# Optimization experiments

Measured on AMD Instinct MI355X. Metric: run time of the kernel, lower is better.

Reference implementation:

```python
import jax, jax.numpy as jnp
import numpy as np

B_, T_, IDIM, D, H, FF, L, MAXLEN = 8, 512, 1799, 256, 4, 2048, 16, 1000
DK = D // H


def _ln(x, g, b, eps=1e-12):
    m = jnp.mean(x, axis=-1, keepdims=True)
    v = jnp.mean((x - m) ** 2, axis=-1, keepdims=True)
    return (x - m) * jax.lax.rsqrt(v + eps) * g + b


def setup_inputs() -> dict:
    key = jax.random.key(0)
    ks = jax.random.split(key, 16)
    s = 0.02
    n = lambda k, shape: jax.random.normal(k, shape, jnp.float32) * s
    return {
        'xs': jax.random.normal(ks[0], (B_, T_, IDIM), jnp.float32),
        'masks': jnp.ones((B_, 1, T_), jnp.int32),
        'emb_w': n(ks[1], (D, IDIM)), 'emb_b': jnp.zeros((D,), jnp.float32),
        'emb_g': jnp.ones((D,), jnp.float32), 'emb_beta': jnp.zeros((D,), jnp.float32),
        'pe_k': n(ks[2], (2 * MAXLEN, DK)),
        'Wq': n(ks[3], (L, D, D)), 'bq': jnp.zeros((L, D), jnp.float32),
        'Wk': n(ks[4], (L, D, D)), 'bk': jnp.zeros((L, D), jnp.float32),
        'Wv': n(ks[5], (L, D, D)), 'bv': jnp.zeros((L, D), jnp.float32),
        'Wo': n(ks[6], (L, D, D)), 'bo': jnp.zeros((L, D), jnp.float32),
        'ln1_g': jnp.ones((L, D), jnp.float32), 'ln1_b': jnp.zeros((L, D), jnp.float32),
        'ln2_g': jnp.ones((L, D), jnp.float32), 'ln2_b': jnp.zeros((L, D), jnp.float32),
        'lnk_g': jnp.ones((L, DK), jnp.float32), 'lnk_b': jnp.zeros((L, DK), jnp.float32),
        'W1': n(ks[7], (L, FF, D)), 'b1': jnp.zeros((L, FF), jnp.float32),
        'W2': n(ks[8], (L, D, FF)), 'b2': jnp.zeros((L, D), jnp.float32),
        'after_g': jnp.ones((D,), jnp.float32), 'after_b': jnp.zeros((D,), jnp.float32),
    }


def reference(xs, masks, emb_w, emb_b, emb_g, emb_beta, pe_k, Wq, bq, Wk, bk, Wv, bv, Wo, bo,
              ln1_g, ln1_b, ln2_g, ln2_b, lnk_g, lnk_b, W1, b1, W2, b2, after_g, after_b):
    # embed: Linear -> LayerNorm -> (Dropout=id) -> ReLU
    x = jax.nn.relu(_ln(xs @ emb_w.T + emb_b, emb_g, emb_beta))  # [B,T,D]
    # relative position table gather: pos_k [T,T,DK]
    pos = jnp.arange(T_)
    rel = jnp.clip(pos[:, None] - pos[None, :], -MAXLEN, MAXLEN - 1) + MAXLEN
    pos_k = pe_k[rel]
    neg = (masks == 0)[:, None, :, :]  # [B,1,1,T]
    minval = jnp.finfo(x.dtype).min
    scale = 1.0 / np.sqrt(DK).astype(np.float32)

    def block(x, p):
        y = _ln(x, p['ln1_g'], p['ln1_b'])
        pk = _ln(pos_k, p['lnk_g'], p['lnk_b'])  # norm_k applied per layer
        proj = lambda W, b: (y @ W.T + b).reshape(B_, T_, H, DK).transpose(0, 2, 1, 3)
        q = proj(p['Wq'], p['bq'])  # [B,H,T,DK]
        k = proj(p['Wk'], p['bk'])
        v = proj(p['Wv'], p['bv'])
        A = jnp.einsum('bhtd,bhsd->bhts', q, k)
        Bt = jnp.einsum('bhtd,tsd->bhts', q, pk)  # rel-pos bias term
        scores = jnp.where(neg, minval, (A + Bt) * scale)
        attn = jnp.where(neg, 0.0, jax.nn.softmax(scores, axis=-1))
        o = jnp.einsum('bhts,bhsd->bhtd', attn, v)
        o = o.transpose(0, 2, 1, 3).reshape(B_, T_, D)
        x = x + o @ p['Wo'].T + p['bo']
        y2 = _ln(x, p['ln2_g'], p['ln2_b'])
        ff = jax.nn.relu(y2 @ p['W1'].T + p['b1']) @ p['W2'].T + p['b2']
        return x + ff, None

    params = {'Wq': Wq, 'bq': bq, 'Wk': Wk, 'bk': bk, 'Wv': Wv, 'bv': bv, 'Wo': Wo, 'bo': bo,
              'ln1_g': ln1_g, 'ln1_b': ln1_b, 'ln2_g': ln2_g, 'ln2_b': ln2_b,
              'lnk_g': lnk_g, 'lnk_b': lnk_b, 'W1': W1, 'b1': b1, 'W2': W2, 'b2': b2}
    x, _ = jax.lax.scan(block, x, params)
    return _ln(x, after_g, after_b)
```

## Files before the change

### kernel.cpp

```cpp
#include <hip/hip_runtime.h>
#include <cstdint>


typedef __bf16 bf16_t;
typedef bf16_t bf16x4 __attribute__((ext_vector_type(4)));
typedef bf16_t bf16x8 __attribute__((ext_vector_type(8)));
typedef float  f32x4  __attribute__((ext_vector_type(4)));

#define B_    8
#define T_    512
#define IDIM  1799
#define KPAD  1856
#define D_    256
#define H_    4
#define DK    64
#define FF_   2048
#define L_    16
#define NROW  4096
#define PKROWS 2000
#define NBH   32
#define NSA   4

__device__ __forceinline__ f32x4 mfma16(bf16x8 a, bf16x8 b, f32x4 c) {
  return __builtin_amdgcn_mfma_f32_16x16x32_bf16(a, b, c, 0, 0, 0);
}

__device__ __forceinline__ void async_cp16(const void* g, void* l) {
  __builtin_amdgcn_global_load_lds(
      (__attribute__((address_space(1))) void*)(g),
      (__attribute__((address_space(3))) void*)(l), 16, 0, 0);
}

#define WCAT_N (L_ * 768 * 256)
#define WOB_N  (L_ * 256 * 256)
#define W1B_N  (L_ * 2048 * 256)
#define W2B_N  (L_ * 256 * 2048)
#define BCAT_N (L_ * 768)
#define PREP_TOT (WCAT_N + WOB_N + W1B_N + W2B_N + BCAT_N)

__global__ __launch_bounds__(256) void prep_all(
    const float* __restrict__ wq, const float* __restrict__ wk,
    const float* __restrict__ wv, const float* __restrict__ wo,
    const float* __restrict__ w1, const float* __restrict__ w2,
    const float* __restrict__ bq, const float* __restrict__ bk,
    const float* __restrict__ bv, bf16_t* __restrict__ wcat,
    bf16_t* __restrict__ wob, bf16_t* __restrict__ w1b,
    bf16_t* __restrict__ w2b, float* __restrict__ bcat) {
  const int stride = gridDim.x * 256;
  for (int i = blockIdx.x * 256 + threadIdx.x; i < PREP_TOT; i += stride) {
    int j = i;
    if (j < WCAT_N) {
      const int per_l = 768 * 256;
      int l = j / per_l, r = j - l * per_l;
      int n = r >> 8, c = r & 255;
      int sel = n >> 8, nn = n & 255;
      const float* wsrc = (sel == 0) ? wq : (sel == 1) ? wk : wv;
      wcat[j] = (bf16_t)wsrc[((size_t)l * 256 + nn) * 256 + c];
      continue;
    }
    j -= WCAT_N;
    if (j < WOB_N) { wob[j] = (bf16_t)wo[j]; continue; }
    j -= WOB_N;
    if (j < W1B_N) { w1b[j] = (bf16_t)w1[j]; continue; }
    j -= W1B_N;
    if (j < W2B_N) { w2b[j] = (bf16_t)w2[j]; continue; }
    j -= W2B_N;
    {
      int l = j / 768, n = j - l * 768;
      int sel = n >> 8, nn = n & 255;
      const float* bsrc = (sel == 0) ? bq : (sel == 1) ? bk : bv;
      bcat[j] = bsrc[l * 256 + nn];
    }
  }
}

__global__ __launch_bounds__(256) void cvt_pad_row(const float* __restrict__ s,
                                                   bf16_t* __restrict__ d,
                                                   int ksrc, int kdst) {
  const int r = blockIdx.x;
  const float* sr = s + (size_t)r * ksrc;
  bf16_t* dr = d + (size_t)r * kdst;
  for (int k = threadIdx.x; k < kdst; k += 256)
    dr[k] = (k < ksrc) ? (bf16_t)sr[k] : (bf16_t)0.f;
}

__global__ __launch_bounds__(256) void pkn_ln(const float* __restrict__ pe_k,
                                              const float* __restrict__ lnk_g,
                                              const float* __restrict__ lnk_b,
                                              bf16_t* __restrict__ out) {
  const int idx = blockIdx.x * 4 + (threadIdx.x >> 6);
  if (idx >= L_ * PKROWS) return;
  const int lane = threadIdx.x & 63;
  const int l = idx / PKROWS, r = idx - l * PKROWS;
  float v = pe_k[(size_t)r * DK + lane];
  float s = v;
#pragma unroll
  for (int o = 32; o; o >>= 1) s += __shfl_xor(s, o);
  const float mean = s * (1.f / DK);
  const float dx = v - mean;
  float q = dx * dx;
#pragma unroll
  for (int o = 32; o; o >>= 1) q += __shfl_xor(q, o);
  const float rs = rsqrtf(q * (1.f / DK) + 1e-12f);
  out[((size_t)l * PKROWS + r) * DK + lane] =
      (bf16_t)(dx * rs * lnk_g[l * DK + lane] + lnk_b[l * DK + lane]);
}

__global__ __launch_bounds__(256) void ln_rows_f32(const float* __restrict__ src,
                                                   const float* __restrict__ g,
                                                   const float* __restrict__ b,
                                                   float* __restrict__ dst) {
  const int row = blockIdx.x * 4 + (threadIdx.x >> 6);
  const int lane = threadIdx.x & 63;
  const float4 v = ((const float4*)(src + (size_t)row * D_))[lane];
  float s = v.x + v.y + v.z + v.w;
#pragma unroll
  for (int o = 32; o; o >>= 1) s += __shfl_xor(s, o);
  const float mean = s * (1.f / D_);
  const float d0 = v.x - mean, d1 = v.y - mean, d2 = v.z - mean, d3 = v.w - mean;
  float q = d0 * d0 + d1 * d1 + d2 * d2 + d3 * d3;
#pragma unroll
  for (int o = 32; o; o >>= 1) q += __shfl_xor(q, o);
  const float rs = rsqrtf(q * (1.f / D_) + 1e-12f);
  const float4 gg = ((const float4*)g)[lane];
  const float4 bb = ((const float4*)b)[lane];
  ((float4*)(dst + (size_t)row * D_))[lane] =
      make_float4(d0 * rs * gg.x + bb.x, d1 * rs * gg.y + bb.y,
                  d2 * rs * gg.z + bb.z, d3 * rs * gg.w + bb.w);
}

template <int NS, bool WRITE_Y>
__global__ __launch_bounds__(256) void add_combine_ln(
    const float* __restrict__ parts, const float* __restrict__ bias,
    float* __restrict__ x, const float* __restrict__ g,
    const float* __restrict__ b, bf16_t* __restrict__ y) {
  const int row = blockIdx.x * 4 + (threadIdx.x >> 6);
  const int lane = threadIdx.x & 63;
  const size_t idx = (size_t)row * 64 + lane;
  float4 v = ((const float4*)x)[idx];
#pragma unroll
  for (int p = 0; p < NS; ++p) {
    float4 pv = ((const float4*)parts)[(size_t)p * NROW * 64 + idx];
    v.x += pv.x; v.y += pv.y; v.z += pv.z; v.w += pv.w;
  }
  const float4 bi = ((const float4*)bias)[lane];
  v.x += bi.x; v.y += bi.y; v.z += bi.z; v.w += bi.w;
  ((float4*)x)[idx] = v;
  if (WRITE_Y) {
    float s = v.x + v.y + v.z + v.w;
#pragma unroll
    for (int o = 32; o; o >>= 1) s += __shfl_xor(s, o);
    const float mean = s * (1.f / D_);
    const float d0 = v.x - mean, d1 = v.y - mean, d2 = v.z - mean, d3 = v.w - mean;
    float q = d0 * d0 + d1 * d1 + d2 * d2 + d3 * d3;
#pragma unroll
    for (int o = 32; o; o >>= 1) q += __shfl_xor(q, o);
    const float rs = rsqrtf(q * (1.f / D_) + 1e-12f);
    const float4 gg = ((const float4*)g)[lane];
    const float4 bb = ((const float4*)b)[lane];
    bf16x4 o4 = {(bf16_t)(d0 * rs * gg.x + bb.x), (bf16_t)(d1 * rs * gg.y + bb.y),
                 (bf16_t)(d2 * rs * gg.z + bb.z), (bf16_t)(d3 * rs * gg.w + bb.w)};
    ((bf16x4*)y)[idx] = o4;
  }
}

__global__ __launch_bounds__(256) void embed_combine(
    const float* __restrict__ parts, const float* __restrict__ bias,
    const float* __restrict__ g0, const float* __restrict__ b0,
    const float* __restrict__ g1, const float* __restrict__ b1,
    float* __restrict__ x, bf16_t* __restrict__ y) {
  const int row = blockIdx.x * 4 + (threadIdx.x >> 6);
  const int lane = threadIdx.x & 63;
  const size_t idx = (size_t)row * 64 + lane;
  float4 v = ((const float4*)parts)[idx];
#pragma unroll
  for (int p = 1; p < 4; ++p) {
    float4 pv = ((const float4*)parts)[(size_t)p * NROW * 64 + idx];
    v.x += pv.x; v.y += pv.y; v.z += pv.z; v.w += pv.w;
  }
  const float4 bi = ((const float4*)bias)[lane];
  v.x += bi.x; v.y += bi.y; v.z += bi.z; v.w += bi.w;
  float s = v.x + v.y + v.z + v.w;
#pragma unroll
  for (int o = 32; o; o >>= 1) s += __shfl_xor(s, o);
  float mean = s * (1.f / D_);
  float d0 = v.x - mean, d1 = v.y - mean, d2 = v.z - mean, d3 = v.w - mean;
  float q = d0 * d0 + d1 * d1 + d2 * d2 + d3 * d3;
#pragma unroll
  for (int o = 32; o; o >>= 1) q += __shfl_xor(q, o);
  float rs = rsqrtf(q * (1.f / D_) + 1e-12f);
  const float4 gg = ((const float4*)g0)[lane];
  const float4 bb = ((const float4*)b0)[lane];
  float x0 = fmaxf(d0 * rs * gg.x + bb.x, 0.f);
  float x1 = fmaxf(d1 * rs * gg.y + bb.y, 0.f);
  float x2 = fmaxf(d2 * rs * gg.z + bb.z, 0.f);
  float x3 = fmaxf(d3 * rs * gg.w + bb.w, 0.f);
  ((float4*)x)[idx] = make_float4(x0, x1, x2, x3);
  s = x0 + x1 + x2 + x3;
#pragma unroll
  for (int o = 32; o; o >>= 1) s += __shfl_xor(s, o);
  mean = s * (1.f / D_);
  d0 = x0 - mean; d1 = x1 - mean; d2 = x2 - mean; d3 = x3 - mean;
  q = d0 * d0 + d1 * d1 + d2 * d2 + d3 * d3;
#pragma unroll
  for (int o = 32; o; o >>= 1) q += __shfl_xor(q, o);
  rs = rsqrtf(q * (1.f / D_) + 1e-12f);
  const float4 g1v = ((const float4*)g1)[lane];
  const float4 b1v = ((const float4*)b1)[lane];
  bf16x4 o4 = {(bf16_t)(d0 * rs * g1v.x + b1v.x), (bf16_t)(d1 * rs * g1v.y + b1v.y),
               (bf16_t)(d2 * rs * g1v.z + b1v.z), (bf16_t)(d3 * rs * g1v.w + b1v.w)};
  ((bf16x4*)y)[idx] = o4;
}

template <int BM, int BN, int EP, int MINW>
__global__ __launch_bounds__(256, MINW) void gemm_bf16(
    const bf16_t* __restrict__ A, int lda, const bf16_t* __restrict__ B, int ldb,
    const float* __restrict__ bias, void* __restrict__ Cout, int ldc,
    int K, size_t zstride) {
  constexpr int HM = BM / 2, HN = BN / 2;
  constexpr int FM = HM / 16, FN = HN / 16;
  constexpr int CA = (BM * 8) / 256, CB = (BN * 8) / 256;
  __shared__ bf16_t lsA[BM * 64];
  __shared__ bf16_t lsB[BN * 64];
  const int tid = threadIdx.x;
  const int w = tid >> 6, lane = tid & 63;
  const int wm = w >> 1, wn = w & 1;
  const int lanelo = lane & 15, quad = lane >> 4;
  const int wbase = tid & ~63;
  const int m0 = blockIdx.x * BM, n0 = blockIdx.y * BN;
  const int ktiles = K >> 6;
  const int tpz = (ktiles + gridDim.z - 1) / gridDim.z;
  const int kb = blockIdx.z * tpz * 64;
  const int ke = min(K, kb + tpz * 64);
  f32x4 acc[FM][FN] = {};

  for (int kt = kb; kt < ke; kt += 64) {
    __syncthreads();
#pragma unroll
    for (int rr = 0; rr < CA; ++rr) {
      int chunk = rr * 256 + tid;
      int r = chunk >> 3, c8 = chunk & 7;
      int lg = c8 ^ (r & 7);
      async_cp16(A + (size_t)(m0 + r) * lda + kt + lg * 8,
                 lsA + (size_t)(rr * 256 + wbase) * 8);
    }
#pragma unroll
    for (int rr = 0; rr < CB; ++rr) {
      int chunk = rr * 256 + tid;
      int r = chunk >> 3, c8 = chunk & 7;
      int lg = c8 ^ (r & 7);
      async_cp16(B + (size_t)(n0 + r) * ldb + kt + lg * 8,
                 lsB + (size_t)(rr * 256 + wbase) * 8);
    }
    __syncthreads();
    bf16x8 af[FM][2], bfv[FN][2];
#pragma unroll
    for (int i = 0; i < FM; ++i) {
      int r = wm * HM + i * 16 + lanelo;
#pragma unroll
      for (int kk = 0; kk < 2; ++kk)
        af[i][kk] = *(const bf16x8*)(lsA + (size_t)(r * 8 + ((kk * 4 + quad) ^ (r & 7))) * 8);
    }
#pragma unroll
    for (int j = 0; j < FN; ++j) {
      int r = wn * HN + j * 16 + lanelo;
#pragma unroll
      for (int kk = 0; kk < 2; ++kk)
        bfv[j][kk] = *(const bf16x8*)(lsB + (size_t)(r * 8 + ((kk * 4 + quad) ^ (r & 7))) * 8);
    }
#pragma unroll
    for (int kk = 0; kk < 2; ++kk)
#pragma unroll
      for (int i = 0; i < FM; ++i)
#pragma unroll
        for (int j = 0; j < FN; ++j)
          acc[i][j] = mfma16(af[i][kk], bfv[j][kk], acc[i][j]);
  }

#pragma unroll
  for (int i = 0; i < FM; ++i) {
#pragma unroll
    for (int j = 0; j < FN; ++j) {
#pragma unroll
      for (int reg = 0; reg < 4; ++reg) {
        const int m = m0 + wm * HM + i * 16 + quad * 4 + reg;
        const int n = n0 + wn * HN + j * 16 + lanelo;
        const size_t idx = (size_t)m * ldc + n;
        if constexpr (EP == 4) {
          ((float*)Cout + (size_t)blockIdx.z * zstride)[idx] = acc[i][j][reg];
        } else {
          float v = acc[i][j][reg] + bias[n];
          if constexpr (EP == 1) {
            ((bf16_t*)Cout)[idx] = (bf16_t)v;
          } else {
            ((bf16_t*)Cout)[idx] = (bf16_t)fmaxf(v, 0.f);
          }
        }
      }
    }
  }
}

__global__ __launch_bounds__(256, 2) void wo_gemm(
    const bf16_t* __restrict__ Opart, const float* __restrict__ mpart,
    const float* __restrict__ lpart, const bf16_t* __restrict__ B,
    float* __restrict__ Cout, size_t zstride) {
  __shared__ bf16_t lsA[64 * 64];
  __shared__ bf16_t lsB[128 * 64];
  const int tid = threadIdx.x;
  const int w = tid >> 6, lane = tid & 63;
  const int wm = w >> 1, wn = w & 1;
  const int lanelo = lane & 15, quad = lane >> 4;
  const int wbase = tid & ~63;
  const int m0 = blockIdx.x * 64, n0 = blockIdx.y * 128;
  const int z = blockIdx.z;
  const int bb = m0 >> 9, t0 = m0 & 511;
  f32x4 acc[2][4] = {};

  for (int kt = z * 128; kt < z * 128 + 128; kt += 64) {
    __syncthreads();
    const int hh = kt >> 6;
    const int bh = bb * 4 + hh;
#pragma unroll
    for (int rr = 0; rr < 2; ++rr) {
      int chunk = rr * 256 + tid;
      int r = chunk >> 3, c8 = chunk & 7;
      int dk0 = (c8 ^ (r & 7)) * 8;
      int t = t0 + r;
      float mp[NSA], lp[NSA];
      float mmax = -__builtin_inff();
#pragma unroll
      for (int p = 0; p < NSA; ++p) {
        const size_t prow = ((size_t)p * NBH + bh) * T_ + t;
        mp[p] = mpart[prow]; lp[p] = lpart[prow];
        mmax = fmaxf(mmax, mp[p]);
      }
      float e[NSA], denom = 0.f;
#pragma unroll
      for (int p = 0; p < NSA; ++p) {
        e[p] = __expf(mp[p] - mmax);
        denom += lp[p] * e[p];
      }
      const float inv = (denom > 0.f) ? 1.f / denom : 0.f;
      float cv[8] = {};
#pragma unroll
      for (int p = 0; p < NSA; ++p) {
        const float wgt = e[p] * inv;
        bf16x8 op = *(const bf16x8*)(Opart +
            (((size_t)p * NBH + bh) * T_ + t) * 64 + dk0);
#pragma unroll
        for (int i = 0; i < 8; ++i) cv[i] += wgt * (float)op[i];
      }
      bf16x8 rv;
#pragma unroll
      for (int i = 0; i < 8; ++i) rv[i] = (bf16_t)cv[i];
      *(bf16x8*)(lsA + (size_t)chunk * 8) = rv;
    }
#pragma unroll
    for (int rr = 0; rr < 4; ++rr) {
      int chunk = rr * 256 + tid;
      int r = chunk >> 3, c8 = chunk & 7;
      int lg = c8 ^ (r & 7);
      async_cp16(B + (size_t)(n0 + r) * 256 + kt + lg * 8,
                 lsB + (size_t)(rr * 256 + wbase) * 8);
    }
    __syncthreads();
    bf16x8 af[2][2], bfv[4][2];
#pragma unroll
    for (int i = 0; i < 2; ++i) {
      int r = wm * 32 + i * 16 + lanelo;
#pragma unroll
      for (int kk = 0; kk < 2; ++kk)
        af[i][kk] = *(const bf16x8*)(lsA + (size_t)(r * 8 + ((kk * 4 + quad) ^ (r & 7))) * 8);
    }
#pragma unroll
    for (int j = 0; j < 4; ++j) {
      int r = wn * 64 + j * 16 + lanelo;
#pragma unroll
      for (int kk = 0; kk < 2; ++kk)
        bfv[j][kk] = *(const bf16x8*)(lsB + (size_t)(r * 8 + ((kk * 4 + quad) ^ (r & 7))) * 8);
    }
#pragma unroll
    for (int kk = 0; kk < 2; ++kk)
#pragma unroll
      for (int i = 0; i < 2; ++i)
#pragma unroll
        for (int j = 0; j < 4; ++j)
          acc[i][j] = mfma16(af[i][kk], bfv[j][kk], acc[i][j]);
  }

#pragma unroll
  for (int i = 0; i < 2; ++i)
#pragma unroll
    for (int j = 0; j < 4; ++j)
#pragma unroll
      for (int reg = 0; reg < 4; ++reg) {
        const int m = m0 + wm * 32 + i * 16 + quad * 4 + reg;
        const int n = n0 + wn * 64 + j * 16 + lanelo;
        (Cout + (size_t)z * zstride)[(size_t)m * D_ + n] = acc[i][j][reg];
      }
}

__global__ __launch_bounds__(256, 3) void attn_fused(
    const bf16_t* __restrict__ qkv, const bf16_t* __restrict__ pkn,
    const int* __restrict__ masks, bf16_t* __restrict__ Opart,
    float* __restrict__ mpart, float* __restrict__ lpart) {
  __shared__ bf16_t ls_qp[64 * 72];
  __shared__ bf16_t ls_pkr[64 * 196];
  __shared__ bf16_t ls_k[64 * 64];
  __shared__ bf16_t ls_vt[64 * 72];

  const int tid = threadIdx.x, w = tid >> 6, lane = tid & 63;
  const int lanelo = lane & 15, quad = lane >> 4;
  const int wbase = tid & ~63;
  const int t0 = blockIdx.x * 64;
  const int bh = blockIdx.y, bb = bh >> 2, h = bh & 3;
  const int z = blockIdx.z;
  const size_t rowbase = (size_t)bb * T_;
  const int jb = t0 - 128 * z + 873;

#pragma unroll
  for (int rr = 0; rr < 2; ++rr) {
    int chunk = rr * 256 + tid;
    int r = chunk >> 3, c8 = chunk & 7;
    int lg = c8 ^ (r & 7);
    async_cp16(qkv + (rowbase + t0 + r) * 768 + h * 64 + lg * 8,
               ls_qp + (size_t)(rr * 256 + wbase) * 8);
  }
#pragma unroll
  for (int rr = 0; rr < 6; ++rr) {
    int chunk = rr * 256 + tid;
    int r = chunk >> 3, c8 = chunk & 7;
    int lg = c8 ^ (r & 7);
    async_cp16(pkn + (size_t)(jb + r) * DK + lg * 8,
               ls_pkr + (size_t)(rr * 256 + wbase) * 8);
  }
  const int s0_0 = 128 * z;
#pragma unroll
  for (int rr = 0; rr < 2; ++rr) {
    int chunk = rr * 256 + tid;
    int r = chunk >> 3, c8 = chunk & 7;
    int lg = c8 ^ (r & 7);
    async_cp16(qkv + (rowbase + s0_0 + r) * 768 + 256 + h * 64 + lg * 8,
               ls_k + (size_t)(rr * 256 + wbase) * 8);
  }
#pragma unroll
  for (int c = tid; c < 64 * 8; c += 256) {
    int r = c & 63, d0 = (c >> 6) * 8;
    bf16x8 vv = *(const bf16x8*)(qkv + (rowbase + s0_0 + r) * 768 + 512 + h * 64 + d0);
#pragma unroll
    for (int i = 0; i < 8; ++i) ls_vt[(d0 + i) * 72 + r] = vv[i];
  }
  int mk[2][4];
#pragma unroll
  for (int stl = 0; stl < 2; ++stl)
#pragma unroll
    for (int nf = 0; nf < 4; ++nf)
      mk[stl][nf] = masks[bb * T_ + 128 * z + 64 * stl + nf * 16 + lanelo];
  __syncthreads();

  bf16x8 qf[2];
#pragma unroll
  for (int kk = 0; kk < 2; ++kk) {
    int r = w * 16 + lanelo;
    qf[kk] = *(const bf16x8*)(ls_qp + (size_t)(r * 8 + ((kk * 4 + quad) ^ (r & 7))) * 8);
  }
  f32x4 racc[12] = {};
#pragma unroll
  for (int kk = 0; kk < 2; ++kk)
#pragma unroll
    for (int nf = 0; nf < 12; ++nf) {
      int r = nf * 16 + lanelo;
      bf16x8 bj = *(const bf16x8*)(ls_pkr + (size_t)(r * 8 + ((kk * 4 + quad) ^ (r & 7))) * 8);
      racc[nf] = mfma16(qf[kk], bj, racc[nf]);
    }
  __syncthreads();
#pragma unroll
  for (int nf = 0; nf < 12; ++nf)
#pragma unroll
    for (int reg = 0; reg < 4; ++reg)
      ls_pkr[(w * 16 + quad * 4 + reg) * 196 + nf * 16 + lanelo] =
          (bf16_t)racc[nf][reg];

  f32x4 o_acc[4] = {};
  float m_run[4], l_run[4];
#pragma unroll
  for (int i = 0; i < 4; ++i) { m_run[i] = -__builtin_inff(); l_run[i] = 0.f; }

  for (int stl = 0; stl < 2; ++stl) {
    const int s0 = 128 * z + 64 * stl;
    if (stl) {
      __syncthreads();
#pragma unroll
      for (int rr = 0; rr < 2; ++rr) {
        int chunk = rr * 256 + tid;
        int r = chunk >> 3, c8 = chunk & 7;
        int lg = c8 ^ (r & 7);
        async_cp16(qkv + (rowbase + s0 + r) * 768 + 256 + h * 64 + lg * 8,
                   ls_k + (size_t)(rr * 256 + wbase) * 8);
      }
#pragma unroll
      for (int c = tid; c < 64 * 8; c += 256) {
        int r = c & 63, d0 = (c >> 6) * 8;
        bf16x8 vv = *(const bf16x8*)(qkv + (rowbase + s0 + r) * 768 + 512 + h * 64 + d0);
#pragma unroll
        for (int i = 0; i < 8; ++i) ls_vt[(d0 + i) * 72 + r] = vv[i];
      }
      __syncthreads();
    }

    f32x4 sacc[4] = {};
#pragma unroll
    for (int kk = 0; kk < 2; ++kk)
#pragma unroll
      for (int nf = 0; nf < 4; ++nf) {
        int r = nf * 16 + lanelo;
        bf16x8 bk = *(const bf16x8*)(ls_k + (size_t)(r * 8 + ((kk * 4 + quad) ^ (r & 7))) * 8);
        sacc[nf] = mfma16(qf[kk], bk, sacc[nf]);
      }
    float sv[4][4];
#pragma unroll
    for (int nf = 0; nf < 4; ++nf) {
      const int scol = nf * 16 + lanelo;
#pragma unroll
      for (int reg = 0; reg < 4; ++reg) {
        const int trow = w * 16 + quad * 4 + reg;
        const float bt = (float)ls_pkr[trow * 196 + (trow - scol - 64 * stl + 127)];
        sv[nf][reg] = mk[stl][nf] ? (sacc[nf][reg] + bt) * 0.125f : -3.4028235e38f;
      }
    }
    float alpha[4];
#pragma unroll
    for (int reg = 0; reg < 4; ++reg) {
      float bm = fmaxf(fmaxf(sv[0][reg], sv[1][reg]), fmaxf(sv[2][reg], sv[3][reg]));
#pragma unroll
      for (int o = 1; o < 16; o <<= 1) bm = fmaxf(bm, __shfl_xor(bm, o));
      const float mn = fmaxf(m_run[reg], bm);
      alpha[reg] = __expf(m_run[reg] - mn);
      m_run[reg] = mn;
      float rsum = 0.f;
#pragma unroll
      for (int nf = 0; nf < 4; ++nf) {
        float p = __expf(sv[nf][reg] - mn) * (mk[stl][nf] ? 1.f : 0.f);
        sv[nf][reg] = p;
        rsum += p;
      }
#pragma unroll
      for (int o = 1; o < 16; o <<= 1) rsum += __shfl_xor(rsum, o);
      l_run[reg] = l_run[reg] * alpha[reg] + rsum;
    }
#pragma unroll
    for (int nf = 0; nf < 4; ++nf)
#pragma unroll
      for (int reg = 0; reg < 4; ++reg) {
        o_acc[nf][reg] *= alpha[reg];
        ls_qp[(w * 16 + quad * 4 + reg) * 72 + nf * 16 + lanelo] = (bf16_t)sv[nf][reg];
      }
#pragma unroll
    for (int kk = 0; kk < 2; ++kk) {
      bf16x8 ap = *(const bf16x8*)&ls_qp[(w * 16 + lanelo) * 72 + kk * 32 + quad * 8];
#pragma unroll
      for (int nf = 0; nf < 4; ++nf) {
        bf16x8 bv = *(const bf16x8*)&ls_vt[(nf * 16 + lanelo) * 72 + kk * 32 + quad * 8];
        o_acc[nf] = mfma16(ap, bv, o_acc[nf]);
      }
    }
  }

#pragma unroll
  for (int reg = 0; reg < 4; ++reg) {
    const int trow = w * 16 + quad * 4 + reg;
    const size_t prow = ((size_t)z * NBH + bh) * T_ + t0 + trow;
#pragma unroll
    for (int nf = 0; nf < 4; ++nf)
      Opart[prow * 64 + nf * 16 + lanelo] = (bf16_t)o_acc[nf][reg];
    if (lanelo == 0) { mpart[prow] = m_run[reg]; lpart[prow] = l_run[reg]; }
  }
}

extern "C" void kernel_launch(void* const* d_in, const int* in_sizes, int n_in,
                              void* d_out, int out_size, void* d_ws, size_t ws_size,
                              hipStream_t stream) {
  const float* xs       = (const float*)d_in[0];
  const int*   masks    = (const int*)d_in[1];
  const float* emb_w    = (const float*)d_in[2];
  const float* emb_b    = (const float*)d_in[3];
  const float* emb_g    = (const float*)d_in[4];
  const float* emb_beta = (const float*)d_in[5];
  const float* pe_k     = (const float*)d_in[6];
  const float* Wq       = (const float*)d_in[7];
  const float* bq       = (const float*)d_in[8];
  const float* Wk       = (const float*)d_in[9];
  const float* bk       = (const float*)d_in[10];
  const float* Wv       = (const float*)d_in[11];
  const float* bv       = (const float*)d_in[12];
  const float* Wo       = (const float*)d_in[13];
  const float* bo       = (const float*)d_in[14];
  const float* ln1_g    = (const float*)d_in[15];
  const float* ln1_b    = (const float*)d_in[16];
  const float* ln2_g    = (const float*)d_in[17];
  const float* ln2_b    = (const float*)d_in[18];
  const float* lnk_g    = (const float*)d_in[19];
  const float* lnk_b    = (const float*)d_in[20];
  const float* W1       = (const float*)d_in[21];
  const float* b1       = (const float*)d_in[22];
  const float* W2       = (const float*)d_in[23];
  const float* b2       = (const float*)d_in[24];
  const float* after_g  = (const float*)d_in[25];
  const float* after_b  = (const float*)d_in[26];

  char* ws = (char*)d_ws;
  size_t off = 0;
  auto take = [&](size_t bytes) -> void* {
    void* p = ws + off;
    off += (bytes + 255) & ~(size_t)255;
    return p;
  };
  bf16_t* ewb  = (bf16_t*)take((size_t)D_ * KPAD * 2);
  bf16_t* wcat = (bf16_t*)take((size_t)L_ * 768 * D_ * 2);
  float*  bcat = (float*) take((size_t)L_ * 768 * 4);
  bf16_t* wob  = (bf16_t*)take((size_t)L_ * D_ * D_ * 2);
  bf16_t* w1b  = (bf16_t*)take((size_t)L_ * FF_ * D_ * 2);
  bf16_t* w2b  = (bf16_t*)take((size_t)L_ * D_ * FF_ * 2);
  bf16_t* pknb = (bf16_t*)take((size_t)L_ * PKROWS * DK * 2);
  float*  x    = (float*) take((size_t)NROW * D_ * 4);
  bf16_t* y    = (bf16_t*)take((size_t)NROW * D_ * 2);
  bf16_t* qkv  = (bf16_t*)take((size_t)NROW * 768 * 2);
  bf16_t* hbuf = (bf16_t*)take((size_t)NROW * FF_ * 2);
  bf16_t* Opart = (bf16_t*)take((size_t)NSA * NBH * T_ * 64 * 2);
  float*  mpart = (float*)take((size_t)NSA * NBH * T_ * 4);
  float*  lpart = (float*)take((size_t)NSA * NBH * T_ * 4);
  float*  gpart = (float*)take((size_t)4 * NROW * D_ * 4);
  bf16_t* xsb  = hbuf;
  const size_t ZS = (size_t)NROW * D_;

  cvt_pad_row<<<NROW, 256, 0, stream>>>(xs, xsb, IDIM, KPAD);
  cvt_pad_row<<<D_, 256, 0, stream>>>(emb_w, ewb, IDIM, KPAD);
  prep_all<<<4096, 256, 0, stream>>>(Wq, Wk, Wv, Wo, W1, W2, bq, bk, bv,
                                     wcat, wob, w1b, w2b, bcat);
  pkn_ln<<<(L_ * PKROWS) / 4, 256, 0, stream>>>(pe_k, lnk_g, lnk_b, pknb);

  gemm_bf16<128, 128, 4, 2><<<dim3(NROW / 128, D_ / 128, 4), 256, 0, stream>>>(
      xsb, KPAD, ewb, KPAD, nullptr, gpart, D_, KPAD, ZS);
  embed_combine<<<NROW / 4, 256, 0, stream>>>(gpart, emb_b, emb_g, emb_beta,
                                              ln1_g, ln1_b, x, y);

  for (int l = 0; l < L_; ++l) {
    gemm_bf16<64, 128, 1, 3><<<dim3(NROW / 64, 768 / 128), 256, 0, stream>>>(
        y, D_, wcat + (size_t)l * 768 * D_, D_, bcat + l * 768, qkv, 768, D_, 0);
    attn_fused<<<dim3(T_ / 64, NBH, NSA), 256, 0, stream>>>(
        qkv, pknb + (size_t)l * PKROWS * DK, masks, Opart, mpart, lpart);
    wo_gemm<<<dim3(NROW / 64, D_ / 128, 2), 256, 0, stream>>>(
        Opart, mpart, lpart, wob + (size_t)l * D_ * D_, gpart, ZS);
    add_combine_ln<2, true><<<NROW / 4, 256, 0, stream>>>(
        gpart, bo + l * D_, x, ln2_g + l * D_, ln2_b + l * D_, y);
    gemm_bf16<128, 128, 2, 2><<<dim3(NROW / 128, FF_ / 128), 256, 0, stream>>>(
        y, D_, w1b + (size_t)l * FF_ * D_, D_, b1 + l * FF_, hbuf, FF_, D_, 0);
    gemm_bf16<128, 128, 4, 2><<<dim3(NROW / 128, D_ / 128, 4), 256, 0, stream>>>(
        hbuf, FF_, w2b + (size_t)l * D_ * FF_, FF_, nullptr, gpart, D_, FF_, ZS);
    if (l < L_ - 1) {
      add_combine_ln<4, true><<<NROW / 4, 256, 0, stream>>>(
          gpart, b2 + l * D_, x, ln1_g + (l + 1) * D_, ln1_b + (l + 1) * D_, y);
    } else {
      add_combine_ln<4, false><<<NROW / 4, 256, 0, stream>>>(
          gpart, b2 + l * D_, x, nullptr, nullptr, nullptr);
    }
  }
  ln_rows_f32<<<NROW / 4, 256, 0, stream>>>(x, after_g, after_b, (float*)d_out);
}
```

Before: 1.304 ms.

## Vectorize prep conversions, fuse Wo residual add, store split-K partials in bf16

```diff
diff --git a/kernel.cpp b/kernel.cpp
--- a/kernel.cpp
+++ b/kernel.cpp
@@ -36,7 +36,7 @@
 #define W1B_N  (L_ * 2048 * 256)
 #define W2B_N  (L_ * 256 * 2048)
 #define BCAT_N (L_ * 768)
-#define PREP_TOT (WCAT_N + WOB_N + W1B_N + W2B_N + BCAT_N)
+#define PREP8  ((WCAT_N + WOB_N + W1B_N + W2B_N) / 8)
 
 __global__ __launch_bounds__(256) void prep_all(
     const float* __restrict__ wq, const float* __restrict__ wk,
@@ -47,30 +47,38 @@
     bf16_t* __restrict__ wob, bf16_t* __restrict__ w1b,
     bf16_t* __restrict__ w2b, float* __restrict__ bcat) {
   const int stride = gridDim.x * 256;
-  for (int i = blockIdx.x * 256 + threadIdx.x; i < PREP_TOT; i += stride) {
-    int j = i;
+  for (int i8 = blockIdx.x * 256 + threadIdx.x; i8 < PREP8; i8 += stride) {
+    int j = i8 * 8;
+    const float* src;
+    bf16_t* dst;
     if (j < WCAT_N) {
       const int per_l = 768 * 256;
       int l = j / per_l, r = j - l * per_l;
       int n = r >> 8, c = r & 255;
       int sel = n >> 8, nn = n & 255;
       const float* wsrc = (sel == 0) ? wq : (sel == 1) ? wk : wv;
-      wcat[j] = (bf16_t)wsrc[((size_t)l * 256 + nn) * 256 + c];
-      continue;
-    }
-    j -= WCAT_N;
-    if (j < WOB_N) { wob[j] = (bf16_t)wo[j]; continue; }
-    j -= WOB_N;
-    if (j < W1B_N) { w1b[j] = (bf16_t)w1[j]; continue; }
-    j -= W1B_N;
-    if (j < W2B_N) { w2b[j] = (bf16_t)w2[j]; continue; }
-    j -= W2B_N;
-    {
-      int l = j / 768, n = j - l * 768;
-      int sel = n >> 8, nn = n & 255;
-      const float* bsrc = (sel == 0) ? bq : (sel == 1) ? bk : bv;
-      bcat[j] = bsrc[l * 256 + nn];
-    }
+      src = wsrc + ((size_t)l * 256 + nn) * 256 + c;
+      dst = wcat + j;
+    } else {
+      j -= WCAT_N;
+      if (j < WOB_N) { src = wo + j; dst = wob + j; }
+      else {
+        j -= WOB_N;
+        if (j < W1B_N) { src = w1 + j; dst = w1b + j; }
+        else { j -= W1B_N; src = w2 + j; dst = w2b + j; }
+      }
+    }
+    float4 a = ((const float4*)src)[0];
+    float4 b = ((const float4*)src)[1];
+    bf16x8 o = {(bf16_t)a.x, (bf16_t)a.y, (bf16_t)a.z, (bf16_t)a.w,
+                (bf16_t)b.x, (bf16_t)b.y, (bf16_t)b.z, (bf16_t)b.w};
+    *(bf16x8*)dst = o;
+  }
+  for (int i = blockIdx.x * 256 + threadIdx.x; i < BCAT_N; i += stride) {
+    int l = i / 768, n = i - l * 768;
+    int sel = n >> 8, nn = n & 255;
+    const float* bsrc = (sel == 0) ? bq : (sel == 1) ? bk : bv;
+    bcat[i] = bsrc[l * 256 + nn];
   }
 }
 
@@ -80,8 +88,15 @@
   const int r = blockIdx.x;
   const float* sr = s + (size_t)r * ksrc;
   bf16_t* dr = d + (size_t)r * kdst;
-  for (int k = threadIdx.x; k < kdst; k += 256)
-    dr[k] = (k < ksrc) ? (bf16_t)sr[k] : (bf16_t)0.f;
+  for (int k8 = threadIdx.x * 8; k8 < kdst; k8 += 256 * 8) {
+    bf16x8 o;
+#pragma unroll
+    for (int i = 0; i < 8; ++i) {
+      int k = k8 + i;
+      o[i] = (k < ksrc) ? (bf16_t)sr[k] : (bf16_t)0.f;
+    }
+    *(bf16x8*)(dr + k8) = o;
+  }
 }
 
 __global__ __launch_bounds__(256) void pkn_ln(const float* __restrict__ pe_k,
@@ -129,9 +144,33 @@
                   d2 * rs * gg.z + bb.z, d3 * rs * gg.w + bb.w);
 }
 
+__global__ __launch_bounds__(256) void ln_y(const float* __restrict__ x,
+                                            const float* __restrict__ g,
+                                            const float* __restrict__ b,
+                                            bf16_t* __restrict__ y) {
+  const int row = blockIdx.x * 4 + (threadIdx.x >> 6);
+  const int lane = threadIdx.x & 63;
+  const size_t idx = (size_t)row * 64 + lane;
+  const float4 v = ((const float4*)x)[idx];
+  float s = v.x + v.y + v.z + v.w;
+#pragma unroll
+  for (int o = 32; o; o >>= 1) s += __shfl_xor(s, o);
+  const float mean = s * (1.f / D_);
+  const float d0 = v.x - mean, d1 = v.y - mean, d2 = v.z - mean, d3 = v.w - mean;
+  float q = d0 * d0 + d1 * d1 + d2 * d2 + d3 * d3;
+#pragma unroll
+  for (int o = 32; o; o >>= 1) q += __shfl_xor(q, o);
+  const float rs = rsqrtf(q * (1.f / D_) + 1e-12f);
+  const float4 gg = ((const float4*)g)[lane];
+  const float4 bb = ((const float4*)b)[lane];
+  bf16x4 o4 = {(bf16_t)(d0 * rs * gg.x + bb.x), (bf16_t)(d1 * rs * gg.y + bb.y),
+               (bf16_t)(d2 * rs * gg.z + bb.z), (bf16_t)(d3 * rs * gg.w + bb.w)};
+  ((bf16x4*)y)[idx] = o4;
+}
+
 template <int NS, bool WRITE_Y>
-__global__ __launch_bounds__(256) void add_combine_ln(
-    const float* __restrict__ parts, const float* __restrict__ bias,
+__global__ __launch_bounds__(256) void add_combine_lnb(
+    const bf16_t* __restrict__ parts, const float* __restrict__ bias,
     float* __restrict__ x, const float* __restrict__ g,
     const float* __restrict__ b, bf16_t* __restrict__ y) {
   const int row = blockIdx.x * 4 + (threadIdx.x >> 6);
@@ -140,8 +179,9 @@
   float4 v = ((const float4*)x)[idx];
 #pragma unroll
   for (int p = 0; p < NS; ++p) {
-    float4 pv = ((const float4*)parts)[(size_t)p * NROW * 64 + idx];
-    v.x += pv.x; v.y += pv.y; v.z += pv.z; v.w += pv.w;
+    bf16x4 pv = ((const bf16x4*)parts)[(size_t)p * NROW * 64 + idx];
+    v.x += (float)pv[0]; v.y += (float)pv[1];
+    v.z += (float)pv[2]; v.w += (float)pv[3];
   }
   const float4 bi = ((const float4*)bias)[lane];
   v.x += bi.x; v.y += bi.y; v.z += bi.z; v.w += bi.w;
@@ -288,6 +328,9 @@
         const size_t idx = (size_t)m * ldc + n;
         if constexpr (EP == 4) {
           ((float*)Cout + (size_t)blockIdx.z * zstride)[idx] = acc[i][j][reg];
+        } else if constexpr (EP == 5) {
+          ((bf16_t*)Cout + (size_t)blockIdx.z * zstride)[idx] =
+              (bf16_t)acc[i][j][reg];
         } else {
           float v = acc[i][j][reg] + bias[n];
           if constexpr (EP == 1) {
@@ -301,10 +344,10 @@
   }
 }
 
-__global__ __launch_bounds__(256, 2) void wo_gemm(
+__global__ __launch_bounds__(256, 2) void wo_direct(
     const bf16_t* __restrict__ Opart, const float* __restrict__ mpart,
     const float* __restrict__ lpart, const bf16_t* __restrict__ B,
-    float* __restrict__ Cout, size_t zstride) {
+    const float* __restrict__ bo, float* __restrict__ x) {
   __shared__ bf16_t lsA[64 * 64];
   __shared__ bf16_t lsB[128 * 64];
   const int tid = threadIdx.x;
@@ -313,11 +356,10 @@
   const int lanelo = lane & 15, quad = lane >> 4;
   const int wbase = tid & ~63;
   const int m0 = blockIdx.x * 64, n0 = blockIdx.y * 128;
-  const int z = blockIdx.z;
   const int bb = m0 >> 9, t0 = m0 & 511;
   f32x4 acc[2][4] = {};
 
-  for (int kt = z * 128; kt < z * 128 + 128; kt += 64) {
+  for (int kt = 0; kt < 256; kt += 64) {
     __syncthreads();
     const int hh = kt >> 6;
     const int bh = bb * 4 + hh;
@@ -397,7 +439,8 @@
       for (int reg = 0; reg < 4; ++reg) {
         const int m = m0 + wm * 32 + i * 16 + quad * 4 + reg;
         const int n = n0 + wn * 64 + j * 16 + lanelo;
-        (Cout + (size_t)z * zstride)[(size_t)m * D_ + n] = acc[i][j][reg];
+        const size_t idx = (size_t)m * D_ + n;
+        x[idx] = x[idx] + acc[i][j][reg] + bo[n];
       }
 }
 
@@ -631,12 +674,13 @@
   float*  mpart = (float*)take((size_t)NSA * NBH * T_ * 4);
   float*  lpart = (float*)take((size_t)NSA * NBH * T_ * 4);
   float*  gpart = (float*)take((size_t)4 * NROW * D_ * 4);
+  bf16_t* gbart = (bf16_t*)gpart;
   bf16_t* xsb  = hbuf;
   const size_t ZS = (size_t)NROW * D_;
 
   cvt_pad_row<<<NROW, 256, 0, stream>>>(xs, xsb, IDIM, KPAD);
   cvt_pad_row<<<D_, 256, 0, stream>>>(emb_w, ewb, IDIM, KPAD);
-  prep_all<<<4096, 256, 0, stream>>>(Wq, Wk, Wv, Wo, W1, W2, bq, bk, bv,
+  prep_all<<<2048, 256, 0, stream>>>(Wq, Wk, Wv, Wo, W1, W2, bq, bk, bv,
                                      wcat, wob, w1b, w2b, bcat);
   pkn_ln<<<(L_ * PKROWS) / 4, 256, 0, stream>>>(pe_k, lnk_g, lnk_b, pknb);
 
@@ -650,20 +694,19 @@
         y, D_, wcat + (size_t)l * 768 * D_, D_, bcat + l * 768, qkv, 768, D_, 0);
     attn_fused<<<dim3(T_ / 64, NBH, NSA), 256, 0, stream>>>(
         qkv, pknb + (size_t)l * PKROWS * DK, masks, Opart, mpart, lpart);
-    wo_gemm<<<dim3(NROW / 64, D_ / 128, 2), 256, 0, stream>>>(
-        Opart, mpart, lpart, wob + (size_t)l * D_ * D_, gpart, ZS);
-    add_combine_ln<2, true><<<NROW / 4, 256, 0, stream>>>(
-        gpart, bo + l * D_, x, ln2_g + l * D_, ln2_b + l * D_, y);
+    wo_direct<<<dim3(NROW / 64, D_ / 128), 256, 0, stream>>>(
+        Opart, mpart, lpart, wob + (size_t)l * D_ * D_, bo + l * D_, x);
+    ln_y<<<NROW / 4, 256, 0, stream>>>(x, ln2_g + l * D_, ln2_b + l * D_, y);
     gemm_bf16<128, 128, 2, 2><<<dim3(NROW / 128, FF_ / 128), 256, 0, stream>>>(
         y, D_, w1b + (size_t)l * FF_ * D_, D_, b1 + l * FF_, hbuf, FF_, D_, 0);
-    gemm_bf16<128, 128, 4, 2><<<dim3(NROW / 128, D_ / 128, 4), 256, 0, stream>>>(
-        hbuf, FF_, w2b + (size_t)l * D_ * FF_, FF_, nullptr, gpart, D_, FF_, ZS);
+    gemm_bf16<128, 128, 5, 2><<<dim3(NROW / 128, D_ / 128, 4), 256, 0, stream>>>(
+        hbuf, FF_, w2b + (size_t)l * D_ * FF_, FF_, nullptr, gbart, D_, FF_, ZS);
     if (l < L_ - 1) {
-      add_combine_ln<4, true><<<NROW / 4, 256, 0, stream>>>(
-          gpart, b2 + l * D_, x, ln1_g + (l + 1) * D_, ln1_b + (l + 1) * D_, y);
+      add_combine_lnb<4, true><<<NROW / 4, 256, 0, stream>>>(
+          gbart, b2 + l * D_, x, ln1_g + (l + 1) * D_, ln1_b + (l + 1) * D_, y);
     } else {
-      add_combine_ln<4, false><<<NROW / 4, 256, 0, stream>>>(
-          gpart, b2 + l * D_, x, nullptr, nullptr, nullptr);
+      add_combine_lnb<4, false><<<NROW / 4, 256, 0, stream>>>(
+          gbart, b2 + l * D_, x, nullptr, nullptr, nullptr);
     }
   }
   ln_rows_f32<<<NROW / 4, 256, 0, stream>>>(x, after_g, after_b, (float*)d_out);
```

Measured after the change: 1.327 ms. Within noise of the previous version (+1.8%).
